# Kernel optimization log

Measured on AMD Instinct MI355X. Metric: run time of the kernel, lower is better.

## Reference

```python
import jax, jax.numpy as jnp
import numpy as np

H = 512  # hidden_size


def setup_inputs() -> dict:
    key = jax.random.key(0)
    ks = jax.random.split(key, 12)
    B, E, S, V = 64, 512, 400, 50000
    s = 1.0 / np.sqrt(H)
    inp = {
        'embedded': jax.random.normal(ks[0], (B, E), jnp.float32),
        'hidden': jax.random.normal(ks[1], (1, B, H), jnp.float32),
        'encoder_states': jax.random.normal(ks[2], (S, B, H), jnp.float32),
        # GRU params (PyTorch layout: gates ordered r,z,n)
        'w_ih': jax.random.uniform(ks[3], (3 * H, E), jnp.float32, -s, s),
        'w_hh': jax.random.uniform(ks[4], (3 * H, H), jnp.float32, -s, s),
        'b_ih': jax.random.uniform(ks[5], (3 * H,), jnp.float32, -s, s),
        'b_hh': jax.random.uniform(ks[6], (3 * H,), jnp.float32, -s, s),
        # nn.Bilinear(H, H, 1)
        'bilin_w': jax.random.uniform(ks[7], (1, H, H), jnp.float32, -s, s),
        'bilin_b': jax.random.uniform(ks[8], (1,), jnp.float32, -s, s),
        # out: Linear(2H, V)
        'out_w': jax.random.uniform(ks[9], (V, 2 * H), jnp.float32, -1.0 / np.sqrt(2 * H), 1.0 / np.sqrt(2 * H)),
        'out_b': jax.random.uniform(ks[10], (V,), jnp.float32, -1.0 / np.sqrt(2 * H), 1.0 / np.sqrt(2 * H)),
    }
    return inp


def reference(embedded, hidden, encoder_states, w_ih, w_hh, b_ih, b_hh,
              bilin_w, bilin_b, out_w, out_b):
    h0 = hidden[0]                                   # [B, H]
    # --- single-step GRU cell (PyTorch gate order r, z, n) ---
    gi = embedded @ w_ih.T + b_ih                    # [B, 3H]
    gh = h0 @ w_hh.T + b_hh                          # [B, 3H]
    r = jax.nn.sigmoid(gi[:, :H] + gh[:, :H])
    z = jax.nn.sigmoid(gi[:, H:2 * H] + gh[:, H:2 * H])
    n = jnp.tanh(gi[:, 2 * H:] + r * gh[:, 2 * H:])
    h_new = (1.0 - z) * n + z * h0                   # [B, H]
    # --- bilinear attention: energy[s,b] = h_new[b] @ W @ enc[s,b] + bias ---
    tmp = h_new @ bilin_w[0]                         # [B, H]
    energy = jnp.einsum('bh,sbh->sb', tmp, encoder_states) + bilin_b[0]  # [S, B]
    attn = jax.nn.softmax(energy, axis=0)            # softmax over source positions
    context = jnp.einsum('sb,sbh->bh', attn, encoder_states)             # [B, H]
    combined = jnp.concatenate([h_new, context], axis=1)                 # [B, 2H]
    logits = combined @ out_w.T + out_b              # [B, V]
    logp = jax.nn.log_softmax(logits, axis=1)
    return logp, h_new[None], attn[:, :, None]
```

## Files before the change

kernel.cpp:

```cpp
#include <hip/hip_runtime.h>
#include <math.h>

static constexpr int H = 512;
static constexpr int B = 64;
static constexpr int FP = 8;

typedef __bf16 bf16x8 __attribute__((ext_vector_type(8)));
typedef __bf16 bf16x4 __attribute__((ext_vector_type(4)));
typedef float f32x4 __attribute__((ext_vector_type(4)));

__device__ __forceinline__ float sigmoidf_(float x) { return 1.f / (1.f + expf(-x)); }

__global__ __launch_bounds__(256) void gemm_gigh(
    const float* __restrict__ embedded, const float* __restrict__ hidden,
    const float* __restrict__ w_ih, const float* __restrict__ w_hh,
    float* __restrict__ gi, float* __restrict__ gh, int K, int N)
{
    const float* A = blockIdx.y ? hidden : embedded;
    const float* W = blockIdx.y ? w_hh : w_ih;
    float* C       = blockIdx.y ? gh : gi;

    __shared__ __bf16 As[2][64 * 64];
    __shared__ __bf16 Ws[2][64 * 64];

    const int tid  = threadIdx.x;
    const int lane = tid & 63;
    const int wv   = tid >> 6;
    const int n0   = blockIdx.x * 64;
    const int lrow = tid >> 2;
    const int lq   = tid & 3;

    const float* Aptr = A + (size_t)lrow * K + lq * 16;
    const float* Wptr = W + (size_t)(n0 + lrow) * K + lq * 16;

    f32x4 acc[4] = {};
    float4 ra[4], rw[4];
    #pragma unroll
    for (int i = 0; i < 4; ++i) {
        ra[i] = *(const float4*)(Aptr + 4 * i);
        rw[i] = *(const float4*)(Wptr + 4 * i);
    }

    const int ln = lane & 15;
    const int lk = (lane >> 4) << 3;
    const int NT = K >> 6;

    for (int t = 0; t < NT; ++t) {
        __bf16* a_s = As[t & 1];
        __bf16* w_s = Ws[t & 1];
        #pragma unroll
        for (int i = 0; i < 4; ++i) {
            const int off = ((lrow << 6) + lq * 16 + 4 * i) ^ ((lrow & 7) << 3);
            *(bf16x4*)&a_s[off] = bf16x4{ (__bf16)ra[i].x, (__bf16)ra[i].y, (__bf16)ra[i].z, (__bf16)ra[i].w };
            *(bf16x4*)&w_s[off] = bf16x4{ (__bf16)rw[i].x, (__bf16)rw[i].y, (__bf16)rw[i].z, (__bf16)rw[i].w };
        }
        __syncthreads();
        if (t + 1 < NT) {
            const float* Ap = Aptr + (t + 1) * 64;
            const float* Wp = Wptr + (t + 1) * 64;
            #pragma unroll
            for (int i = 0; i < 4; ++i) {
                ra[i] = *(const float4*)(Ap + 4 * i);
                rw[i] = *(const float4*)(Wp + 4 * i);
            }
        }
        bf16x8 bfrag[2];
        #pragma unroll
        for (int ks = 0; ks < 2; ++ks) {
            const int row = wv * 16 + ln;
            const int off = ((row << 6) + ks * 32 + lk) ^ ((row & 7) << 3);
            bfrag[ks] = *(bf16x8*)&w_s[off];
        }
        #pragma unroll
        for (int m = 0; m < 4; ++m) {
            const int row = m * 16 + ln;
            #pragma unroll
            for (int ks = 0; ks < 2; ++ks) {
                const int off = ((row << 6) + ks * 32 + lk) ^ ((row & 7) << 3);
                bf16x8 afrag = *(bf16x8*)&a_s[off];
                acc[m] = __builtin_amdgcn_mfma_f32_16x16x32_bf16(afrag, bfrag[ks], acc[m], 0, 0, 0);
            }
        }
    }

    const int col = n0 + wv * 16 + ln;
    #pragma unroll
    for (int m = 0; m < 4; ++m) {
        const int rbase = m * 16 + (lane >> 4) * 4;
        #pragma unroll
        for (int j = 0; j < 4; ++j)
            C[(size_t)(rbase + j) * N + col] = acc[m][j];
    }
}

__global__ __launch_bounds__(512) void gru_gates(
    const float* __restrict__ gi, const float* __restrict__ gh,
    const float* __restrict__ b_ih, const float* __restrict__ b_hh,
    const float* __restrict__ h0, float* __restrict__ hnew,
    __bf16* __restrict__ cbf)
{
    const int b = blockIdx.x;
    const int h = threadIdx.x;
    const size_t o = (size_t)b * 3 * H;
    const float r = sigmoidf_(gi[o + h] + gh[o + h] + b_ih[h] + b_hh[h]);
    const float z = sigmoidf_(gi[o + H + h] + gh[o + H + h] + b_ih[H + h] + b_hh[H + h]);
    const float n = tanhf(gi[o + 2 * H + h] + b_ih[2 * H + h]
                          + r * (gh[o + 2 * H + h] + b_hh[2 * H + h]));
    const float hn = (1.f - z) * n + z * h0[(size_t)b * H + h];
    hnew[(size_t)b * H + h] = hn;
    cbf[(size_t)b * 2 * H + h] = (__bf16)hn;
}

__global__ __launch_bounds__(256) void gemm_a64_kn(
    const float* __restrict__ A, const float* __restrict__ W,
    float* __restrict__ C, int K, int N, int ldc)
{
    __shared__ float As[64][68];
    __shared__ float Bs[64][68];
    const int tid = threadIdx.x;
    const int n0 = blockIdx.x * 64;
    const int tv = tid & 15;
    const int tb = tid >> 4;
    const int lrow = tid >> 2;
    const int lk0  = (tid & 3) * 16;

    float acc[4][4] = {{0.f, 0.f, 0.f, 0.f}};

    for (int kc = 0; kc < K; kc += 64) {
        #pragma unroll
        for (int i = 0; i < 4; ++i) {
            const float4 a = *(const float4*)(A + (size_t)lrow * K + kc + lk0 + 4 * i);
            As[lk0 + 4 * i + 0][lrow] = a.x;
            As[lk0 + 4 * i + 1][lrow] = a.y;
            As[lk0 + 4 * i + 2][lrow] = a.z;
            As[lk0 + 4 * i + 3][lrow] = a.w;
        }
        {
            const int v  = tid & 63;
            const int kg = tid >> 6;
            #pragma unroll
            for (int i = 0; i < 16; ++i) {
                const int kk = kg * 16 + i;
                Bs[kk][v] = (n0 + v < N) ? W[(size_t)(kc + kk) * N + n0 + v] : 0.f;
            }
        }
        __syncthreads();
        #pragma unroll 16
        for (int kk = 0; kk < 64; ++kk) {
            const float4 a = *(const float4*)&As[kk][tb * 4];
            const float4 b = *(const float4*)&Bs[kk][tv * 4];
            acc[0][0] += a.x * b.x; acc[0][1] += a.x * b.y; acc[0][2] += a.x * b.z; acc[0][3] += a.x * b.w;
            acc[1][0] += a.y * b.x; acc[1][1] += a.y * b.y; acc[1][2] += a.y * b.z; acc[1][3] += a.y * b.w;
            acc[2][0] += a.z * b.x; acc[2][1] += a.z * b.y; acc[2][2] += a.z * b.z; acc[2][3] += a.z * b.w;
            acc[3][0] += a.w * b.x; acc[3][1] += a.w * b.y; acc[3][2] += a.w * b.z; acc[3][3] += a.w * b.w;
        }
        __syncthreads();
    }
    #pragma unroll
    for (int i = 0; i < 4; ++i) {
        const int bb = tb * 4 + i;
        #pragma unroll
        for (int j = 0; j < 4; ++j) {
            const int n = n0 + tv * 4 + j;
            if (n < N) C[(size_t)bb * ldc + n] = acc[i][j];
        }
    }
}

__global__ __launch_bounds__(256) void flash4(
    const float* __restrict__ tmp, const float* __restrict__ enc,
    const float* __restrict__ bilin_b, float* __restrict__ energy,
    float* __restrict__ ctxp, float* __restrict__ mp, float* __restrict__ lp,
    int S)
{
    const int b  = blockIdx.x;
    const int p  = blockIdx.y;
    const int wv = threadIdx.x >> 6;
    const int ln = threadIdx.x & 63;
    const int chunk = (S + FP - 1) / FP;
    const int s0 = p * chunk;
    int s1 = s0 + chunk; if (s1 > S) s1 = S;
    const int k0 = ln * 8;

    const float4 t0 = *(const float4*)(tmp + (size_t)b * H + k0);
    const float4 t1 = *(const float4*)(tmp + (size_t)b * H + k0 + 4);
    const float bb = bilin_b[0];

    float m = -1e30f, l = 0.f;
    float4 c0 = {0.f, 0.f, 0.f, 0.f}, c1 = {0.f, 0.f, 0.f, 0.f};

    for (int s = s0 + wv; s < s1; s += 4) {
        const float* e = enc + ((size_t)s * B + b) * H + k0;
        const float4 e0 = *(const float4*)(e);
        const float4 e1 = *(const float4*)(e + 4);
        float d = e0.x * t0.x + e0.y * t0.y + e0.z * t0.z + e0.w * t0.w
                + e1.x * t1.x + e1.y * t1.y + e1.z * t1.z + e1.w * t1.w;
        #pragma unroll
        for (int off = 32; off; off >>= 1) d += __shfl_xor(d, off);
        const float E = d + bb;
        if (ln == 0) energy[(size_t)s * B + b] = E;
        const float mn = fmaxf(m, E);
        const float sc = expf(m - mn);
        const float w  = expf(E - mn);
        l = l * sc + w;
        c0.x = c0.x * sc + w * e0.x; c0.y = c0.y * sc + w * e0.y;
        c0.z = c0.z * sc + w * e0.z; c0.w = c0.w * sc + w * e0.w;
        c1.x = c1.x * sc + w * e1.x; c1.y = c1.y * sc + w * e1.y;
        c1.z = c1.z * sc + w * e1.z; c1.w = c1.w * sc + w * e1.w;
        m = mn;
    }

    __shared__ float sctx[4][H];
    __shared__ float sm4[4], sl4[4];
    *(float4*)&sctx[wv][k0]     = c0;
    *(float4*)&sctx[wv][k0 + 4] = c1;
    if (ln == 0) { sm4[wv] = m; sl4[wv] = l; }
    __syncthreads();
    const float bm = fmaxf(fmaxf(sm4[0], sm4[1]), fmaxf(sm4[2], sm4[3]));
    const float s0c = expf(sm4[0] - bm), s1c = expf(sm4[1] - bm);
    const float s2c = expf(sm4[2] - bm), s3c = expf(sm4[3] - bm);
    const float bl = sl4[0] * s0c + sl4[1] * s1c + sl4[2] * s2c + sl4[3] * s3c;
    for (int e = threadIdx.x; e < H; e += 256) {
        const float v = sctx[0][e] * s0c + sctx[1][e] * s1c
                      + sctx[2][e] * s2c + sctx[3][e] * s3c;
        ctxp[((size_t)b * FP + p) * H + e] = v;
    }
    if (threadIdx.x == 0) { mp[b * FP + p] = bm; lp[b * FP + p] = bl; }
}

__global__ __launch_bounds__(256) void attn_combine(
    const float* __restrict__ mp, const float* __restrict__ lp,
    const float* __restrict__ ctxp, const float* __restrict__ energy,
    __bf16* __restrict__ cbf, float* __restrict__ attn, int S)
{
    const int b = blockIdx.x;
    const int t = threadIdx.x;
    __shared__ float sc_[FP];
    __shared__ float sM, sInvL;
    if (t == 0) {
        float M = -1e30f;
        #pragma unroll
        for (int p = 0; p < FP; ++p) M = fmaxf(M, mp[b * FP + p]);
        float L = 0.f;
        #pragma unroll
        for (int p = 0; p < FP; ++p) {
            const float s = expf(mp[b * FP + p] - M);
            sc_[p] = s;
            L += lp[b * FP + p] * s;
        }
        sM = M; sInvL = 1.f / L;
    }
    __syncthreads();
    const float M = sM, invL = sInvL;

    for (int e = t; e < H; e += 256) {
        float acc = 0.f;
        #pragma unroll
        for (int p = 0; p < FP; ++p)
            acc += ctxp[((size_t)b * FP + p) * H + e] * sc_[p];
        cbf[(size_t)b * 2 * H + H + e] = (__bf16)(acc * invL);
    }
    for (int s = t; s < S; s += 256)
        attn[(size_t)s * B + b] = expf(energy[(size_t)s * B + b] - M) * invL;
}

__global__ __launch_bounds__(256) void gemm_big(
    const __bf16* __restrict__ Ab,
    const float* __restrict__ W,
    const float* __restrict__ bias,
    float* __restrict__ C, float* __restrict__ pm, float* __restrict__ ps,
    int N, int ldc)
{
    constexpr int K = 1024;
    __shared__ __bf16 As[64 * 256];

    const int tid  = threadIdx.x;
    const int lane = tid & 63;
    const int wv   = tid >> 6;
    const int n0   = blockIdx.x * 64 + wv * 16;
    const int ln   = lane & 15;
    const int lk8  = (lane >> 4) << 3;

    int wr = n0 + ln;
    if (wr > N - 1) wr = N - 1;
    const float* wp = W + (size_t)wr * K + lk8;

    f32x4 acc[4] = {};

    for (int q = 0; q < 4; ++q) {
        bf16x8 av[8];
        #pragma unroll
        for (int i = 0; i < 8; ++i) {
            const int c   = tid + (i << 8);
            const int row = c >> 5;
            const int eb  = (c & 31) << 3;
            av[i] = *(const bf16x8*)(Ab + (size_t)row * K + q * 256 + eb);
        }
        f32x4 wb[16];
        const float* wq = wp + q * 256;
        #pragma unroll
        for (int ks = 0; ks < 8; ++ks) {
            wb[2 * ks]     = __builtin_nontemporal_load((const f32x4*)(wq + ks * 32));
            wb[2 * ks + 1] = __builtin_nontemporal_load((const f32x4*)(wq + ks * 32 + 4));
        }
        __syncthreads();
        #pragma unroll
        for (int i = 0; i < 8; ++i) {
            const int c   = tid + (i << 8);
            const int row = c >> 5;
            const int eb  = (c & 31) << 3;
            const int off = (row << 8) + (eb ^ ((row & 7) << 3));
            *(bf16x8*)&As[off] = av[i];
        }
        __syncthreads();
        #pragma unroll
        for (int ks = 0; ks < 8; ++ks) {
            const f32x4 w0 = wb[2 * ks];
            const f32x4 w1 = wb[2 * ks + 1];
            const bf16x8 bw = { (__bf16)w0.x, (__bf16)w0.y, (__bf16)w0.z, (__bf16)w0.w,
                                (__bf16)w1.x, (__bf16)w1.y, (__bf16)w1.z, (__bf16)w1.w };
            #pragma unroll
            for (int m = 0; m < 4; ++m) {
                const int row = m * 16 + ln;
                const int off = (row << 8) + ((ks * 32 + lk8) ^ ((row & 7) << 3));
                const bf16x8 af = *(const bf16x8*)&As[off];
                acc[m] = __builtin_amdgcn_mfma_f32_16x16x32_bf16(af, bw, acc[m], 0, 0, 0);
            }
        }
    }

    const int col = n0 + ln;
    const float bv = (col < N) ? bias[col] : 0.f;
    __syncthreads();
    float* wmf = (float*)As;
    float* wsf = wmf + 256;

    #pragma unroll
    for (int m = 0; m < 4; ++m) {
        #pragma unroll
        for (int j = 0; j < 4; ++j) {
            const int rr = m * 16 + (lane >> 4) * 4 + j;
            float v = acc[m][j] + bv;
            if (col < N) C[(size_t)rr * ldc + col] = v;
            else v = -1e30f;
            float vm = v;
            #pragma unroll
            for (int off = 8; off; off >>= 1) vm = fmaxf(vm, __shfl_xor(vm, off));
            float e = (col < N) ? expf(v - vm) : 0.f;
            #pragma unroll
            for (int off = 8; off; off >>= 1) e += __shfl_xor(e, off);
            if (ln == 0) {
                wmf[wv * 64 + rr] = vm;
                wsf[wv * 64 + rr] = e;
            }
        }
    }
    __syncthreads();
    if (tid < 64) {
        const float m0 = wmf[tid], m1 = wmf[64 + tid], m2 = wmf[128 + tid], m3 = wmf[192 + tid];
        const float bm = fmaxf(fmaxf(m0, m1), fmaxf(m2, m3));
        const float bs = wsf[tid] * expf(m0 - bm) + wsf[64 + tid] * expf(m1 - bm)
                       + wsf[128 + tid] * expf(m2 - bm) + wsf[192 + tid] * expf(m3 - bm);
        pm[(size_t)tid * gridDim.x + blockIdx.x] = bm;
        ps[(size_t)tid * gridDim.x + blockIdx.x] = bs;
    }
}

__global__ __launch_bounds__(256) void lsm_rowcombine(
    const float* __restrict__ pm, const float* __restrict__ ps,
    float* __restrict__ c, int NB)
{
    const int row = blockIdx.x;
    const int t = threadIdx.x;
    const float* pmr = pm + (size_t)row * NB;
    const float* psr = ps + (size_t)row * NB;
    __shared__ float sm_[4], ss_[4];

    float m = -1e30f;
    for (int i = t; i < NB; i += 256) m = fmaxf(m, pmr[i]);
    #pragma unroll
    for (int off = 32; off; off >>= 1) m = fmaxf(m, __shfl_xor(m, off));
    if ((t & 63) == 0) sm_[t >> 6] = m;
    __syncthreads();
    m = fmaxf(fmaxf(sm_[0], sm_[1]), fmaxf(sm_[2], sm_[3]));

    float s = 0.f;
    for (int i = t; i < NB; i += 256) s += psr[i] * expf(pmr[i] - m);
    #pragma unroll
    for (int off = 32; off; off >>= 1) s += __shfl_xor(s, off);
    if ((t & 63) == 0) ss_[t >> 6] = s;
    __syncthreads();
    if (t == 0) c[row] = m + logf(ss_[0] + ss_[1] + ss_[2] + ss_[3]);
}

__global__ __launch_bounds__(256) void lsm_apply(
    float* __restrict__ logits, const float* __restrict__ c, int V)
{
    const int b = blockIdx.y;
    const int i = blockIdx.x * 256 + threadIdx.x;
    const int V4 = V >> 2;
    if (i >= V4) return;
    float4* row = (float4*)(logits + (size_t)b * V);
    float4 v = row[i];
    const float cb = c[b];
    v.x -= cb; v.y -= cb; v.z -= cb; v.w -= cb;
    row[i] = v;
}

extern "C" void kernel_launch(void* const* d_in, const int* in_sizes, int n_in,
                              void* d_out, int out_size, void* d_ws, size_t ws_size,
                              hipStream_t stream)
{
    const float* embedded = (const float*)d_in[0];
    const float* hidden   = (const float*)d_in[1];
    const float* enc      = (const float*)d_in[2];
    const float* w_ih     = (const float*)d_in[3];
    const float* w_hh     = (const float*)d_in[4];
    const float* b_ih     = (const float*)d_in[5];
    const float* b_hh     = (const float*)d_in[6];
    const float* bilin_w  = (const float*)d_in[7];
    const float* bilin_b  = (const float*)d_in[8];
    const float* out_w    = (const float*)d_in[9];
    const float* out_b    = (const float*)d_in[10];
    float* out = (float*)d_out;

    const int S = in_sizes[2] / (B * H);
    const int V = in_sizes[9] / (2 * H);
    const int NB = (V + 63) / 64;

    float* logp = out;
    float* hnew = out + (size_t)B * V;
    float* attn = hnew + (size_t)B * H;

    float* ws     = (float*)d_ws;
    float* gi     = ws;
    float* gh     = gi + (size_t)B * 3 * H;
    float* tmp    = gh + (size_t)B * 3 * H;
    float* energy = tmp + (size_t)B * H;
    float* ctxp   = energy + (size_t)S * B;
    float* mp     = ctxp + (size_t)B * FP * H;
    float* lp     = mp + (size_t)B * FP;
    float* pm     = lp + (size_t)B * FP;
    float* ps     = pm + (size_t)64 * NB;
    float* cb     = ps + (size_t)64 * NB;
    __bf16* cbf   = (__bf16*)(cb + 64);

    gemm_gigh<<<dim3(24, 2), 256, 0, stream>>>(embedded, hidden, w_ih, w_hh, gi, gh, H, 3 * H);

    gru_gates<<<B, H, 0, stream>>>(gi, gh, b_ih, b_hh, hidden, hnew, cbf);

    gemm_a64_kn<<<H / 64, 256, 0, stream>>>(hnew, bilin_w, tmp, H, H, H);

    flash4<<<dim3(B, FP), 256, 0, stream>>>(tmp, enc, bilin_b, energy, ctxp, mp, lp, S);

    attn_combine<<<B, 256, 0, stream>>>(mp, lp, ctxp, energy, cbf, attn, S);

    gemm_big<<<NB, 256, 0, stream>>>(cbf, out_w, out_b, logp, pm, ps, V, V);

    lsm_rowcombine<<<B, 256, 0, stream>>>(pm, ps, cb, NB);

    lsm_apply<<<dim3((V / 4 + 255) / 256, B), 256, 0, stream>>>(logp, cb, V);
}
```

Measured before the change: 158.1 us.

## Widen gemm_big tile to 128 columns per block, two MFMA N-tiles per wave

Each wave now computes 32 output columns, two 16-wide MFMA tiles, instead of 16. Each staged A tile in shared memory is therefore reused across twice as many weight rows, and the grid shrinks by half. The weight loads also move from nontemporal register prefetch before the barrier to plain loads inside the compute loop, which may expose global memory latency. The kernel is likely bound by streaming the 200MB fp32 weight matrix, so fewer blocks with serialized loads could reduce memory-level parallelism.

```diff
diff --git a/kernel.cpp b/kernel.cpp
--- a/kernel.cpp
+++ b/kernel.cpp
@@ -277,15 +277,16 @@
     const int tid  = threadIdx.x;
     const int lane = tid & 63;
     const int wv   = tid >> 6;
-    const int n0   = blockIdx.x * 64 + wv * 16;
+    const int n0   = blockIdx.x * 128 + wv * 32;
     const int ln   = lane & 15;
     const int lk8  = (lane >> 4) << 3;
 
-    int wr = n0 + ln;
-    if (wr > N - 1) wr = N - 1;
-    const float* wp = W + (size_t)wr * K + lk8;
-
-    f32x4 acc[4] = {};
+    int wr0 = n0 + ln;       if (wr0 > N - 1) wr0 = N - 1;
+    int wr1 = n0 + 16 + ln;  if (wr1 > N - 1) wr1 = N - 1;
+    const float* wp0 = W + (size_t)wr0 * K + lk8;
+    const float* wp1 = W + (size_t)wr1 * K + lk8;
+
+    f32x4 acc[4][2] = {};
 
     for (int q = 0; q < 4; ++q) {
         bf16x8 av[8];
@@ -295,13 +296,6 @@
             const int row = c >> 5;
             const int eb  = (c & 31) << 3;
             av[i] = *(const bf16x8*)(Ab + (size_t)row * K + q * 256 + eb);
-        }
-        f32x4 wb[16];
-        const float* wq = wp + q * 256;
-        #pragma unroll
-        for (int ks = 0; ks < 8; ++ks) {
-            wb[2 * ks]     = __builtin_nontemporal_load((const f32x4*)(wq + ks * 32));
-            wb[2 * ks + 1] = __builtin_nontemporal_load((const f32x4*)(wq + ks * 32 + 4));
         }
         __syncthreads();
         #pragma unroll
@@ -313,24 +307,33 @@
             *(bf16x8*)&As[off] = av[i];
         }
         __syncthreads();
+        const float* wq0 = wp0 + q * 256;
+        const float* wq1 = wp1 + q * 256;
         #pragma unroll
         for (int ks = 0; ks < 8; ++ks) {
-            const f32x4 w0 = wb[2 * ks];
-            const f32x4 w1 = wb[2 * ks + 1];
-            const bf16x8 bw = { (__bf16)w0.x, (__bf16)w0.y, (__bf16)w0.z, (__bf16)w0.w,
-                                (__bf16)w1.x, (__bf16)w1.y, (__bf16)w1.z, (__bf16)w1.w };
+            const float4 a0 = *(const float4*)(wq0 + ks * 32);
+            const float4 a1 = *(const float4*)(wq0 + ks * 32 + 4);
+            const float4 b0 = *(const float4*)(wq1 + ks * 32);
+            const float4 b1 = *(const float4*)(wq1 + ks * 32 + 4);
+            const bf16x8 bw0 = { (__bf16)a0.x, (__bf16)a0.y, (__bf16)a0.z, (__bf16)a0.w,
+                                 (__bf16)a1.x, (__bf16)a1.y, (__bf16)a1.z, (__bf16)a1.w };
+            const bf16x8 bw1 = { (__bf16)b0.x, (__bf16)b0.y, (__bf16)b0.z, (__bf16)b0.w,
+                                 (__bf16)b1.x, (__bf16)b1.y, (__bf16)b1.z, (__bf16)b1.w };
             #pragma unroll
             for (int m = 0; m < 4; ++m) {
                 const int row = m * 16 + ln;
                 const int off = (row << 8) + ((ks * 32 + lk8) ^ ((row & 7) << 3));
                 const bf16x8 af = *(const bf16x8*)&As[off];
-                acc[m] = __builtin_amdgcn_mfma_f32_16x16x32_bf16(af, bw, acc[m], 0, 0, 0);
+                acc[m][0] = __builtin_amdgcn_mfma_f32_16x16x32_bf16(af, bw0, acc[m][0], 0, 0, 0);
+                acc[m][1] = __builtin_amdgcn_mfma_f32_16x16x32_bf16(af, bw1, acc[m][1], 0, 0, 0);
             }
         }
     }
 
-    const int col = n0 + ln;
-    const float bv = (col < N) ? bias[col] : 0.f;
+    const int col0 = n0 + ln;
+    const int col1 = n0 + 16 + ln;
+    const float bv0 = (col0 < N) ? bias[col0] : 0.f;
+    const float bv1 = (col1 < N) ? bias[col1] : 0.f;
     __syncthreads();
     float* wmf = (float*)As;
     float* wsf = wmf + 256;
@@ -340,13 +343,16 @@
         #pragma unroll
         for (int j = 0; j < 4; ++j) {
             const int rr = m * 16 + (lane >> 4) * 4 + j;
-            float v = acc[m][j] + bv;
-            if (col < N) C[(size_t)rr * ldc + col] = v;
-            else v = -1e30f;
-            float vm = v;
+            float v0 = acc[m][0][j] + bv0;
+            float v1 = acc[m][1][j] + bv1;
+            if (col0 < N) C[(size_t)rr * ldc + col0] = v0;
+            else v0 = -1e30f;
+            if (col1 < N) C[(size_t)rr * ldc + col1] = v1;
+            else v1 = -1e30f;
+            float vm = fmaxf(v0, v1);
             #pragma unroll
             for (int off = 8; off; off >>= 1) vm = fmaxf(vm, __shfl_xor(vm, off));
-            float e = (col < N) ? expf(v - vm) : 0.f;
+            float e = ((col0 < N) ? expf(v0 - vm) : 0.f) + ((col1 < N) ? expf(v1 - vm) : 0.f);
             #pragma unroll
             for (int off = 8; off; off >>= 1) e += __shfl_xor(e, off);
             if (ln == 0) {
@@ -426,7 +432,7 @@
 
     const int S = in_sizes[2] / (B * H);
     const int V = in_sizes[9] / (2 * H);
-    const int NB = (V + 63) / 64;
+    const int NB = (V + 127) / 128;
 
     float* logp = out;
     float* hnew = out + (size_t)B * V;
```

Measured after the change: 157.8 us. Within noise of the previous version (-0.2%).
